# Kernel optimization log

Hardware: AMD Instinct MI355X
Metric: run time of the kernel (lower is better)

The kernel has to match this reference:

```python
import jax, jax.numpy as jnp
import numpy as np

B, SEQ, C, H, OVERLAP, G, K, D = 16, 8192, 192, 16, 4, 6, 1024, 8
FIX = H * C                      # 3072 (proj_ratio = 1.0, no in/out proj)
DG = (FIX * OVERLAP) // G        # 2048, per-group dim
W = SEQ // H                     # 512 time frames
T = W // OVERLAP                 # 128 grouped frames


def _l2norm(x, eps=1e-12):
    return x / jnp.clip(jnp.linalg.norm(x, axis=-1, keepdims=True), eps)


def setup_inputs() -> dict:
    key = jax.random.key(0)
    k0, k1, k2, k3 = jax.random.split(key, 4)
    z = jax.random.normal(k0, (B, SEQ, C), jnp.float32)
    # stacked per-group parameters (all groups have equal dim DG)
    proj_down = jax.random.normal(k1, (G, DG, D), jnp.float32) * (DG ** -0.5)
    proj_up = jax.random.normal(k2, (G, D, DG), jnp.float32) * (D ** -0.5)
    codebooks = jax.random.normal(k3, (G, K, D), jnp.float32)
    return {"z": z, "proj_down": proj_down, "proj_up": proj_up, "codebooks": codebooks}


def reference(z, proj_down, proj_up, codebooks):
    # --- pre_process: 'b (h w) c -> b w (c h)' then fold overlap ---
    zz = z.reshape(B, H, W, C)                      # b h w c
    zz = jnp.transpose(zz, (0, 2, 3, 1))            # b w c h
    zz = zz.reshape(B, W, FIX)                      # b w (c h)
    zz = zz.reshape(B, T, OVERLAP * FIX)            # fold overlap frames
    zg = zz.reshape(B, T, G, DG)                    # split into G groups

    # --- per-group codebook VQ (vectorized over G) ---
    z_e = jnp.einsum('btgd,gde->btge', zg, proj_down)           # (B,T,G,D)
    sim = jnp.einsum('btge,gke->btgk', _l2norm(z_e), _l2norm(codebooks))
    code = jnp.argmax(sim, axis=-1)                             # (B,T,G)
    gidx = jnp.arange(G)[None, None, :]
    z_q = codebooks[gidx, code]                                 # (B,T,G,D)

    # per-batch-element losses, mean over (T, D) per group, averaged over groups
    commitment = jnp.mean((z_e - jax.lax.stop_gradient(z_q)) ** 2, axis=(1, 3)).mean(axis=1)
    codebook_l = jnp.mean((jax.lax.stop_gradient(z_e) - z_q) ** 2, axis=(1, 3)).mean(axis=1)

    # straight-through estimator + up projection
    z_q_st = z_e + jax.lax.stop_gradient(z_q - z_e)
    z_up = jnp.einsum('btge,ged->btgd', z_q_st, proj_up)        # (B,T,G,DG)
    z_up = z_up.reshape(B, T, OVERLAP * FIX)

    # --- post_process: unfold overlap, 'b w (c h) -> b (h w) c' ---
    out = z_up.reshape(B, W, FIX)                   # b w (c h)
    out = out.reshape(B, W, C, H)
    out = jnp.transpose(out, (0, 3, 1, 2))          # b h w c
    out = out.reshape(B, SEQ, C)
    return out, commitment, codebook_l
```

## Files before the change

### kernel.cpp

```cpp
#include <hip/hip_runtime.h>
#include <math.h>

#define B_ 16
#define SEQ_ 8192
#define C_ 192
#define H_ 16
#define OV_ 4
#define G_ 6
#define K_ 1024
#define D_ 8
#define DG_ 2048
#define W_ 512
#define T_ 128
#define TT 4
#define OUT_ELEMS (B_ * SEQ_ * C_)



__global__ __launch_bounds__(256) void vq_prep(
    const float* __restrict__ pd, const float* __restrict__ pu,
    const float* __restrict__ cb,
    float* __restrict__ pd_p, float* __restrict__ pu_p,
    double* __restrict__ cbn, float* __restrict__ loss_slots)
{
  int i = blockIdx.x * 256 + threadIdx.x;
  if (i < 98304) {
    int e = i & 7, dp = (i >> 3) & 2047, g = i >> 14;
    int h = dp >> 7, ul = dp & 127, d = (ul << 4) + h;
    pd_p[i] = pd[(g << 14) + (d << 3) + e];
  } else if (i < 196608) {
    int i2 = i - 98304;
    int dp = i2 & 2047, e = (i2 >> 11) & 7, g = i2 >> 14;
    int h = dp >> 7, ul = dp & 127, d = (ul << 4) + h;
    pu_p[i2] = pu[(g << 14) + (e << 11) + d];
  } else if (i < 202752) {
    int j = i - 196608;
    const float* row = cb + (j << 3);
    double ss = 0.0;
    #pragma unroll
    for (int e = 0; e < 8; ++e) { double x = (double)row[e]; ss += x * x; }
    double inv = 1.0 / fmax(sqrt(ss), 1e-12);
    #pragma unroll
    for (int e = 0; e < 8; ++e) cbn[(j << 3) + e] = (double)row[e] * inv;
  } else if (i < 202784) {
    loss_slots[i - 202752] = 0.0f;
  }
}

__global__ __launch_bounds__(256) void vq_main(
    const float* __restrict__ z, const float* __restrict__ cb,
    const float* __restrict__ pd_p, const float* __restrict__ pu_p,
    const double* __restrict__ cbn,
    float* __restrict__ out, float* __restrict__ loss_slots)
{
  __shared__ __align__(16) float zs[TT * DG_];
  __shared__ double ze_d[TT * 8];
  __shared__ float  zq_s[TT * 8];
  __shared__ double wr_s[4][TT];
  __shared__ int    wr_k[4][TT];
  __shared__ float  lossv[TT];

  const int tid = threadIdx.x;
  const int tc  = blockIdx.x;
  const int g   = blockIdx.y;
  const int b   = blockIdx.z;

  const float* zb = z + (size_t)b * (SEQ_ * C_);

  #pragma unroll
  for (int t = 0; t < TT; ++t) {
    int wbase = (tc * TT + t) * OV_;
    #pragma unroll
    for (int j = 0; j < 2; ++j) {
      int v  = j * 256 + tid;
      int h  = v >> 5;
      int ul = (v & 31) << 2;
      int u  = (g << 7) + ul;
      int o  = (u * 683) >> 17;
      int c  = u - o * 192;
      const float4 val = *(const float4*)(zb + (h * 512 + wbase + o) * 192 + c);
      *(float4*)(&zs[t * DG_ + (h << 7) + ul]) = val;
    }
  }
  __syncthreads();

  double acc[TT][8];
  #pragma unroll
  for (int t = 0; t < TT; ++t)
    #pragma unroll
    for (int e = 0; e < 8; ++e) acc[t][e] = 0.0;

  #pragma unroll
  for (int i = 0; i < 8; ++i) {
    int dp = i * 256 + tid;
    const float4 p0 = *(const float4*)(pd_p + ((((g << 11) + dp) << 3)));
    const float4 p1 = *(const float4*)(pd_p + ((((g << 11) + dp) << 3) + 4));
    #pragma unroll
    for (int t = 0; t < TT; ++t) {
      double zv = (double)zs[t * DG_ + dp];
      acc[t][0] = fma(zv, (double)p0.x, acc[t][0]);
      acc[t][1] = fma(zv, (double)p0.y, acc[t][1]);
      acc[t][2] = fma(zv, (double)p0.z, acc[t][2]);
      acc[t][3] = fma(zv, (double)p0.w, acc[t][3]);
      acc[t][4] = fma(zv, (double)p1.x, acc[t][4]);
      acc[t][5] = fma(zv, (double)p1.y, acc[t][5]);
      acc[t][6] = fma(zv, (double)p1.z, acc[t][6]);
      acc[t][7] = fma(zv, (double)p1.w, acc[t][7]);
    }
  }

  double* part_d = (double*)zs;
  #pragma unroll
  for (int r = 0; r < 2; ++r) {
    __syncthreads();
    #pragma unroll
    for (int kkl = 0; kkl < 16; ++kkl) {
      int kk = r * 16 + kkl;
      part_d[kkl * 256 + tid] = acc[kk >> 3][kk & 7];
    }
    __syncthreads();
    int kkl = tid >> 4, jj = tid & 15;
    double partial = 0.0;
    #pragma unroll
    for (int s = 0; s < 16; ++s) {
      int p = (s + tid) & 15;
      partial += part_d[kkl * 256 + jj * 16 + p];
    }
    partial += __shfl_down(partial, 8);
    partial += __shfl_down(partial, 4);
    partial += __shfl_down(partial, 2);
    partial += __shfl_down(partial, 1);
    if (jj == 0) ze_d[r * 16 + kkl] = partial;
  }
  __syncthreads();

  double cd[4][8];
  #pragma unroll
  for (int q = 0; q < 4; ++q) {
    const double* cr = cbn + (((g << 10) + (q << 8) + tid) << 3);
    #pragma unroll
    for (int e = 0; e < 8; ++e) cd[q][e] = cr[e];
  }
  double bs[TT]; int bk[TT];
  #pragma unroll
  for (int t = 0; t < TT; ++t) {
    double zr[8];
    #pragma unroll
    for (int e = 0; e < 8; ++e) zr[e] = ze_d[t * 8 + e];
    bs[t] = -1.0e300; bk[t] = 0x7fffffff;
    #pragma unroll
    for (int q = 0; q < 4; ++q) {
      double s = 0.0;
      #pragma unroll
      for (int e = 0; e < 8; ++e) s = fma(zr[e], cd[q][e], s);
      int k = (q << 8) + tid;
      if (s > bs[t]) { bs[t] = s; bk[t] = k; }
    }
  }
  #pragma unroll
  for (int m = 32; m >= 1; m >>= 1) {
    #pragma unroll
    for (int t = 0; t < TT; ++t) {
      double os = __shfl_xor(bs[t], m);
      int    ok = __shfl_xor(bk[t], m);
      if (os > bs[t] || (os == bs[t] && ok < bk[t])) { bs[t] = os; bk[t] = ok; }
    }
  }
  int wv = tid >> 6;
  if ((tid & 63) == 0) {
    #pragma unroll
    for (int t = 0; t < TT; ++t) { wr_s[wv][t] = bs[t]; wr_k[wv][t] = bk[t]; }
  }
  __syncthreads();
  if (tid < TT) {
    int t = tid;
    double s0 = wr_s[0][t]; int k0 = wr_k[0][t];
    #pragma unroll
    for (int w2 = 1; w2 < 4; ++w2) {
      double s1 = wr_s[w2][t]; int k1 = wr_k[w2][t];
      if (s1 > s0 || (s1 == s0 && k1 < k0)) { s0 = s1; k0 = k1; }
    }
    const float* crow = cb + (((g << 10) + k0) << 3);
    double l = 0.0;
    #pragma unroll
    for (int e = 0; e < 8; ++e) {
      float qv = crow[e];
      zq_s[t * 8 + e] = qv;
      double dd = ze_d[t * 8 + e] - (double)qv;
      l = fma(dd, dd, l);
    }
    lossv[t] = (float)l;
  }
  __syncthreads();
  if (tid == 0) {
    float l = (lossv[0] + lossv[1] + lossv[2] + lossv[3]) * (1.0f / (T_ * D_ * G_));
    atomicAdd(loss_slots + b, l);
    atomicAdd(loss_slots + 16 + b, l);
  }

  float zqr[TT][8];
  #pragma unroll
  for (int t = 0; t < TT; ++t)
    #pragma unroll
    for (int e = 0; e < 8; ++e) zqr[t][e] = zq_s[t * 8 + e];

  #pragma unroll
  for (int j = 0; j < 8; ++j) {
    int dp = j * 256 + tid;
    int h = dp >> 7, ul = dp & 127;
    int u = (g << 7) + ul;
    int o = (u * 683) >> 17;
    int c = u - o * 192;
    float pv[8];
    #pragma unroll
    for (int e = 0; e < 8; ++e) pv[e] = pu_p[(g << 14) + (e << 11) + dp];
    size_t base = ((size_t)(b * SEQ_) + h * 512 + tc * (TT * OV_) + o) * 192 + c;
    #pragma unroll
    for (int t = 0; t < TT; ++t) {
      float v = 0.f;
      #pragma unroll
      for (int e = 0; e < 8; ++e) v = fmaf(zqr[t][e], pv[e], v);
      out[base + (size_t)(t * OV_ * 192)] = v;
    }
  }
}

extern "C" void kernel_launch(void* const* d_in, const int* in_sizes, int n_in,
                              void* d_out, int out_size, void* d_ws, size_t ws_size,
                              hipStream_t stream)
{
  const float* z  = (const float*)d_in[0];
  const float* pd = (const float*)d_in[1];
  const float* pu = (const float*)d_in[2];
  const float* cb = (const float*)d_in[3];
  float* out = (float*)d_out;
  float* loss_slots = out + OUT_ELEMS;

  float*  pd_p = (float*)d_ws;
  float*  pu_p = pd_p + 98304;
  double* cbn  = (double*)(pu_p + 98304);

  vq_prep<<<793, 256, 0, stream>>>(pd, pu, cb, pd_p, pu_p, cbn, loss_slots);
  dim3 grid(T_ / TT, G_, B_);
  vq_main<<<grid, 256, 0, stream>>>(z, cb, pd_p, pu_p, cbn, out, loss_slots);
}
```

Measured before the change: 212.4 us.

## Load z directly into registers, skip shared staging, restructure down-projection by time pairs

Drops the shared-memory staging of the z tile. Each thread now loads two float4s per frame straight from global memory and accumulates the down-projection in registers, processing two frames at a time. The per-thread contiguous dp chunk lets it read 4 consecutive pd_p rows as float4s. This removes a large LDS round-trip and a barrier, and halves the accumulator register footprint, which may raise occupancy. In exchange it adds an extra reduction pass per time pair and changes the summation order of the partial sums.

```diff
diff --git a/kernel.cpp b/kernel.cpp
--- a/kernel.cpp
+++ b/kernel.cpp
@@ -53,7 +53,7 @@
     const double* __restrict__ cbn,
     float* __restrict__ out, float* __restrict__ loss_slots)
 {
-  __shared__ __align__(16) float zs[TT * DG_];
+  __shared__ double part_d[16 * 256];
   __shared__ double ze_d[TT * 8];
   __shared__ float  zq_s[TT * 8];
   __shared__ double wr_s[4][TT];
@@ -67,70 +67,71 @@
 
   const float* zb = z + (size_t)b * (SEQ_ * C_);
 
-  #pragma unroll
-  for (int t = 0; t < TT; ++t) {
-    int wbase = (tc * TT + t) * OV_;
+  const int h0  = tid >> 5;
+  const int ul0 = (tid & 31) << 2;
+  const int h1  = h0 + 8;
+  const int dp40 = (h0 << 7) + ul0;
+  const int dp41 = (h1 << 7) + ul0;
+
+  #pragma unroll
+  for (int tp = 0; tp < 2; ++tp) {
+    float4 zf[2][2];
+    #pragma unroll
+    for (int t2 = 0; t2 < 2; ++t2) {
+      const size_t rb = (size_t)((tc * TT + (tp * 2 + t2)) * OV_) * 192 + (g << 7) + ul0;
+      zf[t2][0] = *(const float4*)(zb + (size_t)h0 * (512 * 192) + rb);
+      zf[t2][1] = *(const float4*)(zb + (size_t)h1 * (512 * 192) + rb);
+    }
+
+    double acc2[2][8];
+    #pragma unroll
+    for (int t2 = 0; t2 < 2; ++t2)
+      #pragma unroll
+      for (int e = 0; e < 8; ++e) acc2[t2][e] = 0.0;
+
     #pragma unroll
     for (int j = 0; j < 2; ++j) {
-      int v  = j * 256 + tid;
-      int h  = v >> 5;
-      int ul = (v & 31) << 2;
-      int u  = (g << 7) + ul;
-      int o  = (u * 683) >> 17;
-      int c  = u - o * 192;
-      const float4 val = *(const float4*)(zb + (h * 512 + wbase + o) * 192 + c);
-      *(float4*)(&zs[t * DG_ + (h << 7) + ul]) = val;
-    }
-  }
-  __syncthreads();
-
-  double acc[TT][8];
-  #pragma unroll
-  for (int t = 0; t < TT; ++t)
-    #pragma unroll
-    for (int e = 0; e < 8; ++e) acc[t][e] = 0.0;
-
-  #pragma unroll
-  for (int i = 0; i < 8; ++i) {
-    int dp = i * 256 + tid;
-    const float4 p0 = *(const float4*)(pd_p + ((((g << 11) + dp) << 3)));
-    const float4 p1 = *(const float4*)(pd_p + ((((g << 11) + dp) << 3) + 4));
-    #pragma unroll
-    for (int t = 0; t < TT; ++t) {
-      double zv = (double)zs[t * DG_ + dp];
-      acc[t][0] = fma(zv, (double)p0.x, acc[t][0]);
-      acc[t][1] = fma(zv, (double)p0.y, acc[t][1]);
-      acc[t][2] = fma(zv, (double)p0.z, acc[t][2]);
-      acc[t][3] = fma(zv, (double)p0.w, acc[t][3]);
-      acc[t][4] = fma(zv, (double)p1.x, acc[t][4]);
-      acc[t][5] = fma(zv, (double)p1.y, acc[t][5]);
-      acc[t][6] = fma(zv, (double)p1.z, acc[t][6]);
-      acc[t][7] = fma(zv, (double)p1.w, acc[t][7]);
-    }
-  }
-
-  double* part_d = (double*)zs;
-  #pragma unroll
-  for (int r = 0; r < 2; ++r) {
+      const int dp4 = j ? dp41 : dp40;
+      const float4* pr = (const float4*)(pd_p + (((g << 11) + dp4) << 3));
+      #pragma unroll
+      for (int l = 0; l < 4; ++l) {
+        const float4 pe0 = pr[l * 2];
+        const float4 pe1 = pr[l * 2 + 1];
+        #pragma unroll
+        for (int t2 = 0; t2 < 2; ++t2) {
+          const float* zp = (const float*)&zf[t2][j];
+          const double zv = (double)zp[l];
+          acc2[t2][0] = fma(zv, (double)pe0.x, acc2[t2][0]);
+          acc2[t2][1] = fma(zv, (double)pe0.y, acc2[t2][1]);
+          acc2[t2][2] = fma(zv, (double)pe0.z, acc2[t2][2]);
+          acc2[t2][3] = fma(zv, (double)pe0.w, acc2[t2][3]);
+          acc2[t2][4] = fma(zv, (double)pe1.x, acc2[t2][4]);
+          acc2[t2][5] = fma(zv, (double)pe1.y, acc2[t2][5]);
+          acc2[t2][6] = fma(zv, (double)pe1.z, acc2[t2][6]);
+          acc2[t2][7] = fma(zv, (double)pe1.w, acc2[t2][7]);
+        }
+      }
+    }
+
     __syncthreads();
     #pragma unroll
-    for (int kkl = 0; kkl < 16; ++kkl) {
-      int kk = r * 16 + kkl;
-      part_d[kkl * 256 + tid] = acc[kk >> 3][kk & 7];
-    }
+    for (int t2 = 0; t2 < 2; ++t2)
+      #pragma unroll
+      for (int e = 0; e < 8; ++e)
+        part_d[((t2 << 3) + e) * 256 + tid] = acc2[t2][e];
     __syncthreads();
-    int kkl = tid >> 4, jj = tid & 15;
+    const int slot = tid >> 4, jj = tid & 15;
     double partial = 0.0;
     #pragma unroll
     for (int s = 0; s < 16; ++s) {
       int p = (s + tid) & 15;
-      partial += part_d[kkl * 256 + jj * 16 + p];
+      partial += part_d[slot * 256 + jj * 16 + p];
     }
     partial += __shfl_down(partial, 8);
     partial += __shfl_down(partial, 4);
     partial += __shfl_down(partial, 2);
     partial += __shfl_down(partial, 1);
-    if (jj == 0) ze_d[r * 16 + kkl] = partial;
+    if (jj == 0) ze_d[(tp << 4) + slot] = partial;
   }
   __syncthreads();
 
```

Result: slower. 264.0 us (+24.3%).
